# Kernel tuning notes

Hardware: AMD Instinct MI355X
Metric: run time of the kernel (lower is better)

Reference implementation:

```python
import jax, jax.numpy as jnp
import numpy as np

B, C, W, H = 4, 256, 64, 64
CQ = C // 8


def setup_inputs() -> dict:
    key = jax.random.key(0)
    ks = jax.random.split(key, 8)
    s = 1.0 / np.sqrt(C)
    return {
        "x": jax.random.normal(ks[0], (B, C, W, H), dtype=jnp.float32),
        "Wq": jax.random.normal(ks[1], (CQ, C), dtype=jnp.float32) * s,
        "bq": jnp.zeros((CQ,), dtype=jnp.float32),
        "Wk": jax.random.normal(ks[2], (CQ, C), dtype=jnp.float32) * s,
        "bk": jnp.zeros((CQ,), dtype=jnp.float32),
        "Wv": jax.random.normal(ks[3], (C, C), dtype=jnp.float32) * s,
        "bv": jnp.zeros((C,), dtype=jnp.float32),
        "gamma": jnp.zeros((1,), dtype=jnp.float32),
    }


def reference(x, Wq, bq, Wk, bk, Wv, bv, gamma):
    b, c, w, h = x.shape
    n = w * h
    xf = x.reshape(b, c, n)  # [B, C, N] flattened spatial
    # 1x1 convs are channel-wise linear maps
    q = jnp.einsum("dc,bcn->bnd", Wq, xf) + bq  # [B, N, C//8]
    k = jnp.einsum("dc,bcn->bdn", Wk, xf) + bk[None, :, None]  # [B, C//8, N]
    v = jnp.einsum("dc,bcn->bdn", Wv, xf) + bv[None, :, None]  # [B, C, N]
    attn = jax.nn.softmax(jnp.einsum("bnd,bdm->bnm", q, k), axis=-1)  # [B, N, N]
    # out[b, c, n] = sum_m v[b, c, m] * attn[b, n, m]
    out = jnp.einsum("bdm,bnm->bdn", v, attn).reshape(b, c, w, h)
    return gamma[0] * out + x
```

## Files before the change

kernel.cpp:

```cpp
#include <hip/hip_runtime.h>
#include <hip/hip_bf16.h>

#define CC 256
#define NN 4096
#define CQ 32
#define LOG2E 1.4426950408889634f

using short8 = __attribute__((ext_vector_type(8))) short;
using f32x4  = __attribute__((ext_vector_type(4))) float;

static __device__ __forceinline__ short f2bf(float f) {
  __hip_bfloat16 h = __float2bfloat16(f);
  return *reinterpret_cast<short*>(&h);
}

__global__ __launch_bounds__(256) void prep_kernel(
    const float* __restrict__ Wq, const float* __restrict__ Wk,
    const float* __restrict__ Wv, __hip_bfloat16* __restrict__ Wf)
{
  int t = blockIdx.x*256 + threadIdx.x;
  int lane = t & 63, frag = t >> 6;
  int tile = frag >> 3, kc = frag & 7;
  int l15 = lane & 15, quad = lane >> 4;
  int R = tile*16 + l15;
  int k0 = kc*32 + quad*8;
  const float* src;
  if (R < 32)       src = Wq + (size_t)R*CC + k0;
  else if (R < 64)  src = Wk + (size_t)(R-32)*CC + k0;
  else              src = Wv + (size_t)(R-64)*CC + k0;
  float4 a = *(const float4*)(src);
  float4 c = *(const float4*)(src + 4);
  short8 o;
  o[0]=f2bf(a.x); o[1]=f2bf(a.y); o[2]=f2bf(a.z); o[3]=f2bf(a.w);
  o[4]=f2bf(c.x); o[5]=f2bf(c.y); o[6]=f2bf(c.z); o[7]=f2bf(c.w);
  *reinterpret_cast<short8*>(reinterpret_cast<short*>(Wf) + (size_t)t*8) = o;
}

__global__ __launch_bounds__(512, 2) void qkv_kernel(
    const float* __restrict__ x, const __hip_bfloat16* __restrict__ Wf,
    const float* __restrict__ bq, const float* __restrict__ bk,
    const float* __restrict__ bv,
    __hip_bfloat16* __restrict__ qb, __hip_bfloat16* __restrict__ kb,
    __hip_bfloat16* __restrict__ vb)
{
  const int b  = blockIdx.y;
  const int n0 = blockIdx.x * 64;
  const int tid = threadIdx.x;
  const int lane = tid & 63;
  const int w = __builtin_amdgcn_readfirstlane(tid >> 6);
  const int l15 = lane & 15, quad = lane >> 4;

  __shared__ __align__(16) short Xs[64][264];
  __shared__ __align__(16) short Vr[8][16][72];

  const int sn = tid & 63, cg8 = tid >> 6;
  const float* xcol = x + (size_t)b*CC*NN + n0 + sn;
#pragma unroll
  for (int it = 0; it < 4; it++) {
    int cbase = it*64 + cg8*8;
    float v[8];
#pragma unroll
    for (int j = 0; j < 8; j++) v[j] = xcol[(size_t)(cbase + j)*NN];
    short8 sv;
#pragma unroll
    for (int j = 0; j < 8; j++) sv[j] = f2bf(v[j]);
    *reinterpret_cast<short8*>(&Xs[sn][cbase]) = sv;
  }
  __syncthreads();

  const short* wfp = reinterpret_cast<const short*>(Wf);

#define QKV_TILE(T) { \
    const int t_ = (T); \
    short8 Af[8]; \
    _Pragma("unroll") \
    for (int kc = 0; kc < 8; kc++) \
      Af[kc] = *(const short8*)(wfp + ((size_t)(t_*8 + kc)*64 + lane)*8); \
    f32x4 ac0 = {0.f,0.f,0.f,0.f}, ac1 = {0.f,0.f,0.f,0.f}; \
    f32x4 ac2 = {0.f,0.f,0.f,0.f}, ac3 = {0.f,0.f,0.f,0.f}; \
    _Pragma("unroll") \
    for (int kc = 0; kc < 8; kc++) { \
      short8 B0 = *(const short8*)(&Xs[     l15][kc*32 + quad*8]); \
      short8 B1 = *(const short8*)(&Xs[16 + l15][kc*32 + quad*8]); \
      short8 B2 = *(const short8*)(&Xs[32 + l15][kc*32 + quad*8]); \
      short8 B3 = *(const short8*)(&Xs[48 + l15][kc*32 + quad*8]); \
      ac0 = __builtin_amdgcn_mfma_f32_16x16x32_bf16(Af[kc], B0, ac0, 0,0,0); \
      ac1 = __builtin_amdgcn_mfma_f32_16x16x32_bf16(Af[kc], B1, ac1, 0,0,0); \
      ac2 = __builtin_amdgcn_mfma_f32_16x16x32_bf16(Af[kc], B2, ac2, 0,0,0); \
      ac3 = __builtin_amdgcn_mfma_f32_16x16x32_bf16(Af[kc], B3, ac3, 0,0,0); \
    } \
    if (t_ < 2) { \
      int d0 = t_*16; \
      _Pragma("unroll") \
      for (int r = 0; r < 4; r++) { \
        int d = d0 + quad*4 + r; float bb = bq[d]; \
        qb[(size_t)b*NN*CQ + (size_t)(n0      + l15)*CQ + d] = __float2bfloat16(LOG2E*(ac0[r] + bb)); \
        qb[(size_t)b*NN*CQ + (size_t)(n0 + 16 + l15)*CQ + d] = __float2bfloat16(LOG2E*(ac1[r] + bb)); \
        qb[(size_t)b*NN*CQ + (size_t)(n0 + 32 + l15)*CQ + d] = __float2bfloat16(LOG2E*(ac2[r] + bb)); \
        qb[(size_t)b*NN*CQ + (size_t)(n0 + 48 + l15)*CQ + d] = __float2bfloat16(LOG2E*(ac3[r] + bb)); \
      } \
    } else if (t_ < 4) { \
      int d0 = (t_-2)*16; \
      _Pragma("unroll") \
      for (int r = 0; r < 4; r++) { \
        int d = d0 + quad*4 + r; float bb = bk[d]; \
        kb[(size_t)b*NN*CQ + (size_t)(n0      + l15)*CQ + d] = __float2bfloat16(ac0[r] + bb); \
        kb[(size_t)b*NN*CQ + (size_t)(n0 + 16 + l15)*CQ + d] = __float2bfloat16(ac1[r] + bb); \
        kb[(size_t)b*NN*CQ + (size_t)(n0 + 32 + l15)*CQ + d] = __float2bfloat16(ac2[r] + bb); \
        kb[(size_t)b*NN*CQ + (size_t)(n0 + 48 + l15)*CQ + d] = __float2bfloat16(ac3[r] + bb); \
      } \
    } else { \
      int rv0 = (t_-4)*16; \
      _Pragma("unroll") \
      for (int r = 0; r < 4; r++) { \
        float bb = bv[rv0 + quad*4 + r]; \
        Vr[w][quad*4 + r][     l15] = f2bf(ac0[r] + bb); \
        Vr[w][quad*4 + r][16 + l15] = f2bf(ac1[r] + bb); \
        Vr[w][quad*4 + r][32 + l15] = f2bf(ac2[r] + bb); \
        Vr[w][quad*4 + r][48 + l15] = f2bf(ac3[r] + bb); \
      } \
      int row = lane >> 2, cb = (lane & 3)*16; \
      short8 t0 = *(const short8*)(&Vr[w][row][cb]); \
      short8 t1 = *(const short8*)(&Vr[w][row][cb + 8]); \
      *(short8*)(vb + ((size_t)b*CC + rv0 + row)*NN + n0 + cb)     = t0; \
      *(short8*)(vb + ((size_t)b*CC + rv0 + row)*NN + n0 + cb + 8) = t1; \
    } }

  QKV_TILE(2*w);
  QKV_TILE(2*w + 1);
  if (w < 4) { QKV_TILE(16 + w); }
#undef QKV_TILE
}

__global__ __launch_bounds__(512, 2) void attn_kernel(
    const __hip_bfloat16* __restrict__ qb, const __hip_bfloat16* __restrict__ kb,
    const __hip_bfloat16* __restrict__ vb,
    const float* __restrict__ x, const float* __restrict__ gamma,
    float* __restrict__ out)
{
  const int Bk = blockIdx.x;
  const int b = (Bk & 7) >> 1;
  const int n0 = ((Bk >> 3)*2 + (Bk & 1)) * 64;
  const int tid = threadIdx.x;
  const int lane = tid & 63;
  const int w = __builtin_amdgcn_readfirstlane(tid >> 6);
  const int sg = w & 3;
  const int mh = w >> 2;
  const int l15 = lane & 15, quad = lane >> 4;

  __shared__ __align__(16) short Vs[256][72];
  __shared__ __align__(16) short Ps[64][72];
  __shared__ float Lbuf2[2][64];

  const short* qbase = (const short*)qb + (size_t)b*NN*CQ;
  const short* kbase = (const short*)kb + (size_t)b*NN*CQ;
  const short* vbase = (const short*)vb + (size_t)b*CC*NN;

  short8 aq = *(const short8*)(qbase + (size_t)(n0 + sg*16 + l15)*CQ + quad*8);

  const int vr = tid >> 1, sh = tid & 1;

  short8 vf0, vf1, vf2, vf3, kf0, kf1;
#pragma unroll
  for (int j = 0; j < 4; j++) {
    short8 t = *(const short8*)(vbase + (size_t)vr*NN + sh*32 + j*8);
    if (j == 0) vf0 = t; else if (j == 1) vf1 = t; else if (j == 2) vf2 = t; else vf3 = t;
  }
  kf0 = *(const short8*)(kbase + (size_t)(mh*32 +      l15)*CQ + quad*8);
  kf1 = *(const short8*)(kbase + (size_t)(mh*32 + 16 + l15)*CQ + quad*8);
  *(short8*)(&Vs[vr][sh*32 +  0]) = vf0;
  *(short8*)(&Vs[vr][sh*32 +  8]) = vf1;
  *(short8*)(&Vs[vr][sh*32 + 16]) = vf2;
  *(short8*)(&Vs[vr][sh*32 + 24]) = vf3;

  f32x4 acc[4][4];
#pragma unroll
  for (int cg = 0; cg < 4; cg++)
#pragma unroll
    for (int ng = 0; ng < 4; ng++) acc[cg][ng] = (f32x4){0.f,0.f,0.f,0.f};
  float lsum[4] = {0.f,0.f,0.f,0.f};

  __syncthreads();

  for (int T = 0; T < 64; T++) {
    short8 nv0, nv1, nv2, nv3, nk0, nk1;
    if (T < 63) {
      const short* vp = vbase + (size_t)vr*NN + (T+1)*64 + sh*32;
      nv0 = *(const short8*)(vp);
      nv1 = *(const short8*)(vp + 8);
      nv2 = *(const short8*)(vp + 16);
      nv3 = *(const short8*)(vp + 24);
      nk0 = *(const short8*)(kbase + (size_t)((T+1)*64 + mh*32 +      l15)*CQ + quad*8);
      nk1 = *(const short8*)(kbase + (size_t)((T+1)*64 + mh*32 + 16 + l15)*CQ + quad*8);
    }

    f32x4 z = {0.f,0.f,0.f,0.f};
    f32x4 S0 = __builtin_amdgcn_mfma_f32_16x16x32_bf16(aq, kf0, z, 0,0,0);
    f32x4 S1 = __builtin_amdgcn_mfma_f32_16x16x32_bf16(aq, kf1, z, 0,0,0);
#pragma unroll
    for (int r = 0; r < 4; r++) {
      float e0 = __builtin_amdgcn_exp2f(S0[r]);
      float e1 = __builtin_amdgcn_exp2f(S1[r]);
      lsum[r] += e0 + e1;
      Ps[sg*16 + quad*4 + r][mh*32 +      l15] = f2bf(e0);
      Ps[sg*16 + quad*4 + r][mh*32 + 16 + l15] = f2bf(e1);
    }
    __syncthreads();

    short8 ap0 = *(const short8*)(&Ps[     l15][mh*32 + quad*8]);
    short8 ap1 = *(const short8*)(&Ps[16 + l15][mh*32 + quad*8]);
    short8 ap2 = *(const short8*)(&Ps[32 + l15][mh*32 + quad*8]);
    short8 ap3 = *(const short8*)(&Ps[48 + l15][mh*32 + quad*8]);
#pragma unroll
    for (int cg = 0; cg < 4; cg++) {
      short8 av = *(const short8*)(&Vs[sg*64 + cg*16 + l15][mh*32 + quad*8]);
      acc[cg][0] = __builtin_amdgcn_mfma_f32_16x16x32_bf16(av, ap0, acc[cg][0], 0,0,0);
      acc[cg][1] = __builtin_amdgcn_mfma_f32_16x16x32_bf16(av, ap1, acc[cg][1], 0,0,0);
      acc[cg][2] = __builtin_amdgcn_mfma_f32_16x16x32_bf16(av, ap2, acc[cg][2], 0,0,0);
      acc[cg][3] = __builtin_amdgcn_mfma_f32_16x16x32_bf16(av, ap3, acc[cg][3], 0,0,0);
    }
    __syncthreads();

    if (T < 63) {
      *(short8*)(&Vs[vr][sh*32 +  0]) = nv0;
      *(short8*)(&Vs[vr][sh*32 +  8]) = nv1;
      *(short8*)(&Vs[vr][sh*32 + 16]) = nv2;
      *(short8*)(&Vs[vr][sh*32 + 24]) = nv3;
      kf0 = nk0; kf1 = nk1;
    }
  }

#pragma unroll
  for (int r = 0; r < 4; r++) {
    float s = lsum[r];
    s += __shfl_xor(s, 1); s += __shfl_xor(s, 2);
    s += __shfl_xor(s, 4); s += __shfl_xor(s, 8);
    if (l15 == 0) Lbuf2[mh][sg*16 + quad*4 + r] = s;
  }

  float* poolf = reinterpret_cast<float*>(&Vs[0][0]);
  __syncthreads();
#pragma unroll
  for (int g = 0; g < 2; g++) {
    if (mh == 1 && (sg >> 1) == g) {
#pragma unroll
      for (int cg = 0; cg < 4; cg++)
#pragma unroll
        for (int ng = 0; ng < 4; ng++)
#pragma unroll
          for (int r = 0; r < 4; r++)
            poolf[(sg & 1)*4096 + (cg*16 + quad*4 + r)*64 + ng*16 + l15] = acc[cg][ng][r];
    }
    __syncthreads();
    if (mh == 0 && (sg >> 1) == g) {
#pragma unroll
      for (int cg = 0; cg < 4; cg++)
#pragma unroll
        for (int ng = 0; ng < 4; ng++)
#pragma unroll
          for (int r = 0; r < 4; r++)
            acc[cg][ng][r] += poolf[(sg & 1)*4096 + (cg*16 + quad*4 + r)*64 + ng*16 + l15];
    }
    __syncthreads();
  }

  if (mh == 0) {
    const float gm = gamma[0];
    float Lv[4];
#pragma unroll
    for (int ng = 0; ng < 4; ng++)
      Lv[ng] = 1.0f / (Lbuf2[0][ng*16 + l15] + Lbuf2[1][ng*16 + l15]);
#pragma unroll
    for (int cg = 0; cg < 4; cg++) {
#pragma unroll
      for (int ng = 0; ng < 4; ng++) {
#pragma unroll
        for (int r = 0; r < 4; r++) {
          size_t idx = ((size_t)b*CC + sg*64 + cg*16 + quad*4 + r)*NN + n0 + ng*16 + l15;
          out[idx] = gm * acc[cg][ng][r] * Lv[ng] + x[idx];
        }
      }
    }
  }
}

extern "C" void kernel_launch(void* const* d_in, const int* in_sizes, int n_in,
                              void* d_out, int out_size, void* d_ws, size_t ws_size,
                              hipStream_t stream) {
  const float* x     = (const float*)d_in[0];
  const float* Wq    = (const float*)d_in[1];
  const float* bq    = (const float*)d_in[2];
  const float* Wk    = (const float*)d_in[3];
  const float* bk    = (const float*)d_in[4];
  const float* Wv    = (const float*)d_in[5];
  const float* bv    = (const float*)d_in[6];
  const float* gamma = (const float*)d_in[7];
  float* out = (float*)d_out;

  char* ws = (char*)d_ws;
  if (ws_size < (11u << 20)) return;
  __hip_bfloat16* qb = (__hip_bfloat16*)(ws);
  __hip_bfloat16* kb = (__hip_bfloat16*)(ws + (1u << 20));
  __hip_bfloat16* vb = (__hip_bfloat16*)(ws + (2u << 20));
  __hip_bfloat16* Wf = (__hip_bfloat16*)(ws + (10u << 20));

  prep_kernel<<<dim3(40), 256, 0, stream>>>(Wq, Wk, Wv, Wf);
  qkv_kernel<<<dim3(64, 4), 512, 0, stream>>>(x, Wf, bq, bk, bv, qb, kb, vb);
  attn_kernel<<<dim3(256), 512, 0, stream>>>(qb, kb, vb, x, gamma, out);
}
```

Before: 155.1 us.

## Load V fragments directly to registers and double-buffer P to drop a barrier

Each wave now reads its V MFMA operands straight from global memory into registers instead of staging V through shared memory. The P tile is double-buffered in LDS so the exp/score step for tile T+1 overlaps the PV MFMAs for tile T, leaving one barrier per iteration instead of two. The K prefetch is moved two tiles ahead. In exchange, global V loads become strided per lane (rows of NN) and register pressure rises. LDS is reduced to one shared float pool that is reused for the epilogue.

```diff
diff --git a/kernel.cpp b/kernel.cpp
--- a/kernel.cpp
+++ b/kernel.cpp
@@ -148,9 +148,9 @@
   const int mh = w >> 2;
   const int l15 = lane & 15, quad = lane >> 4;
 
-  __shared__ __align__(16) short Vs[256][72];
-  __shared__ __align__(16) short Ps[64][72];
+  __shared__ __align__(16) float poolf[8192];
   __shared__ float Lbuf2[2][64];
+  auto Ps = reinterpret_cast<short (*)[64][72]>(poolf);
 
   const short* qbase = (const short*)qb + (size_t)b*NN*CQ;
   const short* kbase = (const short*)kb + (size_t)b*NN*CQ;
@@ -158,76 +158,93 @@
 
   short8 aq = *(const short8*)(qbase + (size_t)(n0 + sg*16 + l15)*CQ + quad*8);
 
-  const int vr = tid >> 1, sh = tid & 1;
-
-  short8 vf0, vf1, vf2, vf3, kf0, kf1;
-#pragma unroll
-  for (int j = 0; j < 4; j++) {
-    short8 t = *(const short8*)(vbase + (size_t)vr*NN + sh*32 + j*8);
-    if (j == 0) vf0 = t; else if (j == 1) vf1 = t; else if (j == 2) vf2 = t; else vf3 = t;
-  }
-  kf0 = *(const short8*)(kbase + (size_t)(mh*32 +      l15)*CQ + quad*8);
-  kf1 = *(const short8*)(kbase + (size_t)(mh*32 + 16 + l15)*CQ + quad*8);
-  *(short8*)(&Vs[vr][sh*32 +  0]) = vf0;
-  *(short8*)(&Vs[vr][sh*32 +  8]) = vf1;
-  *(short8*)(&Vs[vr][sh*32 + 16]) = vf2;
-  *(short8*)(&Vs[vr][sh*32 + 24]) = vf3;
-
+  const short* vp0 = vbase + (size_t)(sg*64 +      l15)*NN + mh*32 + quad*8;
+  const short* vp1 = vp0 + (size_t)16*NN;
+  const short* vp2 = vp0 + (size_t)32*NN;
+  const short* vp3 = vp0 + (size_t)48*NN;
+  const short* kp0 = kbase + (size_t)(mh*32 +      l15)*CQ + quad*8;
+  const short* kp1 = kbase + (size_t)(mh*32 + 16 + l15)*CQ + quad*8;
+
+  const f32x4 z = {0.f,0.f,0.f,0.f};
   f32x4 acc[4][4];
 #pragma unroll
   for (int cg = 0; cg < 4; cg++)
 #pragma unroll
-    for (int ng = 0; ng < 4; ng++) acc[cg][ng] = (f32x4){0.f,0.f,0.f,0.f};
+    for (int ng = 0; ng < 4; ng++) acc[cg][ng] = z;
   float lsum[4] = {0.f,0.f,0.f,0.f};
 
+  short8 kf0 = *(const short8*)(kp0);
+  short8 kf1 = *(const short8*)(kp1);
+  short8 vf0 = *(const short8*)(vp0);
+  short8 vf1 = *(const short8*)(vp1);
+  short8 vf2 = *(const short8*)(vp2);
+  short8 vf3 = *(const short8*)(vp3);
+  {
+    f32x4 s0 = __builtin_amdgcn_mfma_f32_16x16x32_bf16(aq, kf0, z, 0,0,0);
+    f32x4 s1 = __builtin_amdgcn_mfma_f32_16x16x32_bf16(aq, kf1, z, 0,0,0);
+#pragma unroll
+    for (int r = 0; r < 4; r++) {
+      float e0 = __builtin_amdgcn_exp2f(s0[r]);
+      float e1 = __builtin_amdgcn_exp2f(s1[r]);
+      lsum[r] += e0 + e1;
+      Ps[0][sg*16 + quad*4 + r][mh*32 +      l15] = f2bf(e0);
+      Ps[0][sg*16 + quad*4 + r][mh*32 + 16 + l15] = f2bf(e1);
+    }
+  }
+  kf0 = *(const short8*)(kp0 + 64*CQ);
+  kf1 = *(const short8*)(kp1 + 64*CQ);
   __syncthreads();
 
   for (int T = 0; T < 64; T++) {
-    short8 nv0, nv1, nv2, nv3, nk0, nk1;
+    const int Tn = (T < 63) ? T + 1 : 63;
+    const int Tk = (T < 62) ? T + 2 : 63;
+    short8 nv0 = *(const short8*)(vp0 + Tn*64);
+    short8 nv1 = *(const short8*)(vp1 + Tn*64);
+    short8 nv2 = *(const short8*)(vp2 + Tn*64);
+    short8 nv3 = *(const short8*)(vp3 + Tn*64);
+    short8 nk0 = *(const short8*)(kp0 + (size_t)Tk*64*CQ);
+    short8 nk1 = *(const short8*)(kp1 + (size_t)Tk*64*CQ);
+
+    const int pb = T & 1;
+    short8 ap0 = *(const short8*)(&Ps[pb][     l15][mh*32 + quad*8]);
+    short8 ap1 = *(const short8*)(&Ps[pb][16 + l15][mh*32 + quad*8]);
+    short8 ap2 = *(const short8*)(&Ps[pb][32 + l15][mh*32 + quad*8]);
+    short8 ap3 = *(const short8*)(&Ps[pb][48 + l15][mh*32 + quad*8]);
+
     if (T < 63) {
-      const short* vp = vbase + (size_t)vr*NN + (T+1)*64 + sh*32;
-      nv0 = *(const short8*)(vp);
-      nv1 = *(const short8*)(vp + 8);
-      nv2 = *(const short8*)(vp + 16);
-      nv3 = *(const short8*)(vp + 24);
-      nk0 = *(const short8*)(kbase + (size_t)((T+1)*64 + mh*32 +      l15)*CQ + quad*8);
-      nk1 = *(const short8*)(kbase + (size_t)((T+1)*64 + mh*32 + 16 + l15)*CQ + quad*8);
-    }
-
-    f32x4 z = {0.f,0.f,0.f,0.f};
-    f32x4 S0 = __builtin_amdgcn_mfma_f32_16x16x32_bf16(aq, kf0, z, 0,0,0);
-    f32x4 S1 = __builtin_amdgcn_mfma_f32_16x16x32_bf16(aq, kf1, z, 0,0,0);
-#pragma unroll
-    for (int r = 0; r < 4; r++) {
-      float e0 = __builtin_amdgcn_exp2f(S0[r]);
-      float e1 = __builtin_amdgcn_exp2f(S1[r]);
-      lsum[r] += e0 + e1;
-      Ps[sg*16 + quad*4 + r][mh*32 +      l15] = f2bf(e0);
-      Ps[sg*16 + quad*4 + r][mh*32 + 16 + l15] = f2bf(e1);
-    }
+      f32x4 s0 = __builtin_amdgcn_mfma_f32_16x16x32_bf16(aq, kf0, z, 0,0,0);
+      f32x4 s1 = __builtin_amdgcn_mfma_f32_16x16x32_bf16(aq, kf1, z, 0,0,0);
+#pragma unroll
+      for (int r = 0; r < 4; r++) {
+        float e0 = __builtin_amdgcn_exp2f(s0[r]);
+        float e1 = __builtin_amdgcn_exp2f(s1[r]);
+        lsum[r] += e0 + e1;
+        Ps[pb^1][sg*16 + quad*4 + r][mh*32 +      l15] = f2bf(e0);
+        Ps[pb^1][sg*16 + quad*4 + r][mh*32 + 16 + l15] = f2bf(e1);
+      }
+    }
+
+    acc[0][0] = __builtin_amdgcn_mfma_f32_16x16x32_bf16(vf0, ap0, acc[0][0], 0,0,0);
+    acc[0][1] = __builtin_amdgcn_mfma_f32_16x16x32_bf16(vf0, ap1, acc[0][1], 0,0,0);
+    acc[0][2] = __builtin_amdgcn_mfma_f32_16x16x32_bf16(vf0, ap2, acc[0][2], 0,0,0);
+    acc[0][3] = __builtin_amdgcn_mfma_f32_16x16x32_bf16(vf0, ap3, acc[0][3], 0,0,0);
+    acc[1][0] = __builtin_amdgcn_mfma_f32_16x16x32_bf16(vf1, ap0, acc[1][0], 0,0,0);
+    acc[1][1] = __builtin_amdgcn_mfma_f32_16x16x32_bf16(vf1, ap1, acc[1][1], 0,0,0);
+    acc[1][2] = __builtin_amdgcn_mfma_f32_16x16x32_bf16(vf1, ap2, acc[1][2], 0,0,0);
+    acc[1][3] = __builtin_amdgcn_mfma_f32_16x16x32_bf16(vf1, ap3, acc[1][3], 0,0,0);
+    acc[2][0] = __builtin_amdgcn_mfma_f32_16x16x32_bf16(vf2, ap0, acc[2][0], 0,0,0);
+    acc[2][1] = __builtin_amdgcn_mfma_f32_16x16x32_bf16(vf2, ap1, acc[2][1], 0,0,0);
+    acc[2][2] = __builtin_amdgcn_mfma_f32_16x16x32_bf16(vf2, ap2, acc[2][2], 0,0,0);
+    acc[2][3] = __builtin_amdgcn_mfma_f32_16x16x32_bf16(vf2, ap3, acc[2][3], 0,0,0);
+    acc[3][0] = __builtin_amdgcn_mfma_f32_16x16x32_bf16(vf3, ap0, acc[3][0], 0,0,0);
+    acc[3][1] = __builtin_amdgcn_mfma_f32_16x16x32_bf16(vf3, ap1, acc[3][1], 0,0,0);
+    acc[3][2] = __builtin_amdgcn_mfma_f32_16x16x32_bf16(vf3, ap2, acc[3][2], 0,0,0);
+    acc[3][3] = __builtin_amdgcn_mfma_f32_16x16x32_bf16(vf3, ap3, acc[3][3], 0,0,0);
+
+    vf0 = nv0; vf1 = nv1; vf2 = nv2; vf3 = nv3;
+    kf0 = nk0; kf1 = nk1;
+
     __syncthreads();
-
-    short8 ap0 = *(const short8*)(&Ps[     l15][mh*32 + quad*8]);
-    short8 ap1 = *(const short8*)(&Ps[16 + l15][mh*32 + quad*8]);
-    short8 ap2 = *(const short8*)(&Ps[32 + l15][mh*32 + quad*8]);
-    short8 ap3 = *(const short8*)(&Ps[48 + l15][mh*32 + quad*8]);
-#pragma unroll
-    for (int cg = 0; cg < 4; cg++) {
-      short8 av = *(const short8*)(&Vs[sg*64 + cg*16 + l15][mh*32 + quad*8]);
-      acc[cg][0] = __builtin_amdgcn_mfma_f32_16x16x32_bf16(av, ap0, acc[cg][0], 0,0,0);
-      acc[cg][1] = __builtin_amdgcn_mfma_f32_16x16x32_bf16(av, ap1, acc[cg][1], 0,0,0);
-      acc[cg][2] = __builtin_amdgcn_mfma_f32_16x16x32_bf16(av, ap2, acc[cg][2], 0,0,0);
-      acc[cg][3] = __builtin_amdgcn_mfma_f32_16x16x32_bf16(av, ap3, acc[cg][3], 0,0,0);
-    }
-    __syncthreads();
-
-    if (T < 63) {
-      *(short8*)(&Vs[vr][sh*32 +  0]) = nv0;
-      *(short8*)(&Vs[vr][sh*32 +  8]) = nv1;
-      *(short8*)(&Vs[vr][sh*32 + 16]) = nv2;
-      *(short8*)(&Vs[vr][sh*32 + 24]) = nv3;
-      kf0 = nk0; kf1 = nk1;
-    }
   }
 
 #pragma unroll
@@ -238,7 +255,6 @@
     if (l15 == 0) Lbuf2[mh][sg*16 + quad*4 + r] = s;
   }
 
-  float* poolf = reinterpret_cast<float*>(&Vs[0][0]);
   __syncthreads();
 #pragma unroll
   for (int g = 0; g < 2; g++) {
```

After: 173.4 us. 1.12x slower.

## Double-buffer V and P tiles in LDS to overlap softmax with PV MFMA

Applied to the files above, without the earlier changes.

Splits the V and P shared-memory tiles into two buffers and software-pipelines the loop. Each iteration computes QK^T and exp for the next key tile into the alternate P buffer while running the PV MFMAs on the current one, and the two barriers per iteration become one. This is meant to hide the exp and LDS-store latency and cut barrier stalls. In exchange, LDS use per block roughly doubles, which may lower the number of resident blocks per CU.

```diff
diff --git a/kernel.cpp b/kernel.cpp
--- a/kernel.cpp
+++ b/kernel.cpp
@@ -148,8 +148,8 @@
   const int mh = w >> 2;
   const int l15 = lane & 15, quad = lane >> 4;
 
-  __shared__ __align__(16) short Vs[256][72];
-  __shared__ __align__(16) short Ps[64][72];
+  __shared__ __align__(16) short Vs[2][256][72];
+  __shared__ __align__(16) short Ps[2][64][72];
   __shared__ float Lbuf2[2][64];
 
   const short* qbase = (const short*)qb + (size_t)b*NN*CQ;
@@ -159,75 +159,94 @@
   short8 aq = *(const short8*)(qbase + (size_t)(n0 + sg*16 + l15)*CQ + quad*8);
 
   const int vr = tid >> 1, sh = tid & 1;
-
-  short8 vf0, vf1, vf2, vf3, kf0, kf1;
-#pragma unroll
-  for (int j = 0; j < 4; j++) {
-    short8 t = *(const short8*)(vbase + (size_t)vr*NN + sh*32 + j*8);
-    if (j == 0) vf0 = t; else if (j == 1) vf1 = t; else if (j == 2) vf2 = t; else vf3 = t;
-  }
-  kf0 = *(const short8*)(kbase + (size_t)(mh*32 +      l15)*CQ + quad*8);
-  kf1 = *(const short8*)(kbase + (size_t)(mh*32 + 16 + l15)*CQ + quad*8);
-  *(short8*)(&Vs[vr][sh*32 +  0]) = vf0;
-  *(short8*)(&Vs[vr][sh*32 +  8]) = vf1;
-  *(short8*)(&Vs[vr][sh*32 + 16]) = vf2;
-  *(short8*)(&Vs[vr][sh*32 + 24]) = vf3;
-
+  const short* vrow = vbase + (size_t)vr*NN + sh*32;
+
+  const f32x4 z = {0.f,0.f,0.f,0.f};
   f32x4 acc[4][4];
 #pragma unroll
   for (int cg = 0; cg < 4; cg++)
 #pragma unroll
-    for (int ng = 0; ng < 4; ng++) acc[cg][ng] = (f32x4){0.f,0.f,0.f,0.f};
+    for (int ng = 0; ng < 4; ng++) acc[cg][ng] = z;
   float lsum[4] = {0.f,0.f,0.f,0.f};
 
+  {
+    short8 a0 = *(const short8*)(vrow);
+    short8 a1 = *(const short8*)(vrow + 8);
+    short8 a2 = *(const short8*)(vrow + 16);
+    short8 a3 = *(const short8*)(vrow + 24);
+    *(short8*)(&Vs[0][vr][sh*32 +  0]) = a0;
+    *(short8*)(&Vs[0][vr][sh*32 +  8]) = a1;
+    *(short8*)(&Vs[0][vr][sh*32 + 16]) = a2;
+    *(short8*)(&Vs[0][vr][sh*32 + 24]) = a3;
+  }
+  {
+    short8 k00 = *(const short8*)(kbase + (size_t)(mh*32 +      l15)*CQ + quad*8);
+    short8 k01 = *(const short8*)(kbase + (size_t)(mh*32 + 16 + l15)*CQ + quad*8);
+    f32x4 s0 = __builtin_amdgcn_mfma_f32_16x16x32_bf16(aq, k00, z, 0,0,0);
+    f32x4 s1 = __builtin_amdgcn_mfma_f32_16x16x32_bf16(aq, k01, z, 0,0,0);
+#pragma unroll
+    for (int r = 0; r < 4; r++) {
+      float e0 = __builtin_amdgcn_exp2f(s0[r]);
+      float e1 = __builtin_amdgcn_exp2f(s1[r]);
+      lsum[r] += e0 + e1;
+      Ps[0][sg*16 + quad*4 + r][mh*32 +      l15] = f2bf(e0);
+      Ps[0][sg*16 + quad*4 + r][mh*32 + 16 + l15] = f2bf(e1);
+    }
+  }
+  short8 kf0 = *(const short8*)(kbase + (size_t)(64 + mh*32 +      l15)*CQ + quad*8);
+  short8 kf1 = *(const short8*)(kbase + (size_t)(64 + mh*32 + 16 + l15)*CQ + quad*8);
   __syncthreads();
 
   for (int T = 0; T < 64; T++) {
-    short8 nv0, nv1, nv2, nv3, nk0, nk1;
+    const int cur = T & 1;
+
+    short8 nv0, nv1, nv2, nv3;
     if (T < 63) {
-      const short* vp = vbase + (size_t)vr*NN + (T+1)*64 + sh*32;
+      const short* vp = vrow + (size_t)(T+1)*64;
       nv0 = *(const short8*)(vp);
       nv1 = *(const short8*)(vp + 8);
       nv2 = *(const short8*)(vp + 16);
       nv3 = *(const short8*)(vp + 24);
-      nk0 = *(const short8*)(kbase + (size_t)((T+1)*64 + mh*32 +      l15)*CQ + quad*8);
-      nk1 = *(const short8*)(kbase + (size_t)((T+1)*64 + mh*32 + 16 + l15)*CQ + quad*8);
-    }
-
-    f32x4 z = {0.f,0.f,0.f,0.f};
-    f32x4 S0 = __builtin_amdgcn_mfma_f32_16x16x32_bf16(aq, kf0, z, 0,0,0);
-    f32x4 S1 = __builtin_amdgcn_mfma_f32_16x16x32_bf16(aq, kf1, z, 0,0,0);
-#pragma unroll
-    for (int r = 0; r < 4; r++) {
-      float e0 = __builtin_amdgcn_exp2f(S0[r]);
-      float e1 = __builtin_amdgcn_exp2f(S1[r]);
-      lsum[r] += e0 + e1;
-      Ps[sg*16 + quad*4 + r][mh*32 +      l15] = f2bf(e0);
-      Ps[sg*16 + quad*4 + r][mh*32 + 16 + l15] = f2bf(e1);
-    }
-    __syncthreads();
-
-    short8 ap0 = *(const short8*)(&Ps[     l15][mh*32 + quad*8]);
-    short8 ap1 = *(const short8*)(&Ps[16 + l15][mh*32 + quad*8]);
-    short8 ap2 = *(const short8*)(&Ps[32 + l15][mh*32 + quad*8]);
-    short8 ap3 = *(const short8*)(&Ps[48 + l15][mh*32 + quad*8]);
+    }
+
+    short8 ap0 = *(const short8*)(&Ps[cur][     l15][mh*32 + quad*8]);
+    short8 ap1 = *(const short8*)(&Ps[cur][16 + l15][mh*32 + quad*8]);
+    short8 ap2 = *(const short8*)(&Ps[cur][32 + l15][mh*32 + quad*8]);
+    short8 ap3 = *(const short8*)(&Ps[cur][48 + l15][mh*32 + quad*8]);
+
+    if (T < 63) {
+      f32x4 s0 = __builtin_amdgcn_mfma_f32_16x16x32_bf16(aq, kf0, z, 0,0,0);
+      f32x4 s1 = __builtin_amdgcn_mfma_f32_16x16x32_bf16(aq, kf1, z, 0,0,0);
+#pragma unroll
+      for (int r = 0; r < 4; r++) {
+        float e0 = __builtin_amdgcn_exp2f(s0[r]);
+        float e1 = __builtin_amdgcn_exp2f(s1[r]);
+        lsum[r] += e0 + e1;
+        Ps[cur^1][sg*16 + quad*4 + r][mh*32 +      l15] = f2bf(e0);
+        Ps[cur^1][sg*16 + quad*4 + r][mh*32 + 16 + l15] = f2bf(e1);
+      }
+      const int Tk = (T + 2 <= 63) ? T + 2 : 63;
+      kf0 = *(const short8*)(kbase + (size_t)(Tk*64 + mh*32 +      l15)*CQ + quad*8);
+      kf1 = *(const short8*)(kbase + (size_t)(Tk*64 + mh*32 + 16 + l15)*CQ + quad*8);
+    }
+
 #pragma unroll
     for (int cg = 0; cg < 4; cg++) {
-      short8 av = *(const short8*)(&Vs[sg*64 + cg*16 + l15][mh*32 + quad*8]);
+      short8 av = *(const short8*)(&Vs[cur][sg*64 + cg*16 + l15][mh*32 + quad*8]);
       acc[cg][0] = __builtin_amdgcn_mfma_f32_16x16x32_bf16(av, ap0, acc[cg][0], 0,0,0);
       acc[cg][1] = __builtin_amdgcn_mfma_f32_16x16x32_bf16(av, ap1, acc[cg][1], 0,0,0);
       acc[cg][2] = __builtin_amdgcn_mfma_f32_16x16x32_bf16(av, ap2, acc[cg][2], 0,0,0);
       acc[cg][3] = __builtin_amdgcn_mfma_f32_16x16x32_bf16(av, ap3, acc[cg][3], 0,0,0);
     }
+
+    if (T < 63) {
+      *(short8*)(&Vs[cur^1][vr][sh*32 +  0]) = nv0;
+      *(short8*)(&Vs[cur^1][vr][sh*32 +  8]) = nv1;
+      *(short8*)(&Vs[cur^1][vr][sh*32 + 16]) = nv2;
+      *(short8*)(&Vs[cur^1][vr][sh*32 + 24]) = nv3;
+    }
+
     __syncthreads();
-
-    if (T < 63) {
-      *(short8*)(&Vs[vr][sh*32 +  0]) = nv0;
-      *(short8*)(&Vs[vr][sh*32 +  8]) = nv1;
-      *(short8*)(&Vs[vr][sh*32 + 16]) = nv2;
-      *(short8*)(&Vs[vr][sh*32 + 24]) = nv3;
-      kf0 = nk0; kf1 = nk1;
-    }
   }
 
 #pragma unroll
@@ -238,7 +257,7 @@
     if (l15 == 0) Lbuf2[mh][sg*16 + quad*4 + r] = s;
   }
 
-  float* poolf = reinterpret_cast<float*>(&Vs[0][0]);
+  float* poolf = reinterpret_cast<float*>(&Vs[0][0][0]);
   __syncthreads();
 #pragma unroll
   for (int g = 0; g < 2; g++) {
```

Measured after the change: 174.7 us. 12.7% more time.

## Halve attention query tile to 32 rows with 4-wave blocks and 512 blocks

Applied to the files above, without the earlier changes.

The attention kernel now handles 32 query positions per block with 256 threads instead of 64 with 512, which doubles the grid to 512 blocks. Each wave accumulates 8x2 output tiles covering 128 channels, and the cross-wave reduction drops to a single pass. Padding of the shared V and P rows changes from 72 to 76 to alter the bank mapping. The intent is to give the GPU's many CUs more blocks to schedule. The cost is that each K/V tile is reloaded by twice as many blocks, doubling global/L2 traffic for V.

```diff
diff --git a/kernel.cpp b/kernel.cpp
--- a/kernel.cpp
+++ b/kernel.cpp
@@ -132,7 +132,7 @@
 #undef QKV_TILE
 }
 
-__global__ __launch_bounds__(512, 2) void attn_kernel(
+__global__ __launch_bounds__(256, 2) void attn_kernel(
     const __hip_bfloat16* __restrict__ qb, const __hip_bfloat16* __restrict__ kb,
     const __hip_bfloat16* __restrict__ vb,
     const float* __restrict__ x, const float* __restrict__ gamma,
@@ -140,17 +140,18 @@
 {
   const int Bk = blockIdx.x;
   const int b = (Bk & 7) >> 1;
-  const int n0 = ((Bk >> 3)*2 + (Bk & 1)) * 64;
+  const int nt = (Bk >> 3)*2 + (Bk & 1);
+  const int n0 = nt * 32;
   const int tid = threadIdx.x;
   const int lane = tid & 63;
   const int w = __builtin_amdgcn_readfirstlane(tid >> 6);
-  const int sg = w & 3;
-  const int mh = w >> 2;
+  const int sg = w & 1;
+  const int mh = w >> 1;
   const int l15 = lane & 15, quad = lane >> 4;
 
-  __shared__ __align__(16) short Vs[256][72];
-  __shared__ __align__(16) short Ps[64][72];
-  __shared__ float Lbuf2[2][64];
+  __shared__ __align__(16) short Vs[256][76];
+  __shared__ __align__(16) short Ps[32][76];
+  __shared__ float Lbuf2[2][32];
 
   const short* qbase = (const short*)qb + (size_t)b*NN*CQ;
   const short* kbase = (const short*)kb + (size_t)b*NN*CQ;
@@ -158,43 +159,38 @@
 
   short8 aq = *(const short8*)(qbase + (size_t)(n0 + sg*16 + l15)*CQ + quad*8);
 
-  const int vr = tid >> 1, sh = tid & 1;
-
-  short8 vf0, vf1, vf2, vf3, kf0, kf1;
-#pragma unroll
-  for (int j = 0; j < 4; j++) {
-    short8 t = *(const short8*)(vbase + (size_t)vr*NN + sh*32 + j*8);
-    if (j == 0) vf0 = t; else if (j == 1) vf1 = t; else if (j == 2) vf2 = t; else vf3 = t;
-  }
-  kf0 = *(const short8*)(kbase + (size_t)(mh*32 +      l15)*CQ + quad*8);
-  kf1 = *(const short8*)(kbase + (size_t)(mh*32 + 16 + l15)*CQ + quad*8);
-  *(short8*)(&Vs[vr][sh*32 +  0]) = vf0;
-  *(short8*)(&Vs[vr][sh*32 +  8]) = vf1;
-  *(short8*)(&Vs[vr][sh*32 + 16]) = vf2;
-  *(short8*)(&Vs[vr][sh*32 + 24]) = vf3;
-
-  f32x4 acc[4][4];
-#pragma unroll
-  for (int cg = 0; cg < 4; cg++)
-#pragma unroll
-    for (int ng = 0; ng < 4; ng++) acc[cg][ng] = (f32x4){0.f,0.f,0.f,0.f};
+  const int vr = tid;
+  const short* vrow = vbase + (size_t)vr*NN;
+
+  const f32x4 z = {0.f,0.f,0.f,0.f};
+  f32x4 acc[8][2];
+#pragma unroll
+  for (int cg = 0; cg < 8; cg++)
+#pragma unroll
+    for (int ng = 0; ng < 2; ng++) acc[cg][ng] = z;
   float lsum[4] = {0.f,0.f,0.f,0.f};
 
+  {
+    short8 sv[8];
+#pragma unroll
+    for (int j = 0; j < 8; j++) sv[j] = *(const short8*)(vrow + j*8);
+#pragma unroll
+    for (int j = 0; j < 8; j++) *(short8*)(&Vs[vr][j*8]) = sv[j];
+  }
+  short8 kf0 = *(const short8*)(kbase + (size_t)(mh*32 +      l15)*CQ + quad*8);
+  short8 kf1 = *(const short8*)(kbase + (size_t)(mh*32 + 16 + l15)*CQ + quad*8);
   __syncthreads();
 
   for (int T = 0; T < 64; T++) {
-    short8 nv0, nv1, nv2, nv3, nk0, nk1;
+    short8 nv[8]; short8 nk0, nk1;
     if (T < 63) {
-      const short* vp = vbase + (size_t)vr*NN + (T+1)*64 + sh*32;
-      nv0 = *(const short8*)(vp);
-      nv1 = *(const short8*)(vp + 8);
-      nv2 = *(const short8*)(vp + 16);
-      nv3 = *(const short8*)(vp + 24);
+      const short* vp = vrow + (size_t)(T+1)*64;
+#pragma unroll
+      for (int j = 0; j < 8; j++) nv[j] = *(const short8*)(vp + j*8);
       nk0 = *(const short8*)(kbase + (size_t)((T+1)*64 + mh*32 +      l15)*CQ + quad*8);
       nk1 = *(const short8*)(kbase + (size_t)((T+1)*64 + mh*32 + 16 + l15)*CQ + quad*8);
     }
 
-    f32x4 z = {0.f,0.f,0.f,0.f};
     f32x4 S0 = __builtin_amdgcn_mfma_f32_16x16x32_bf16(aq, kf0, z, 0,0,0);
     f32x4 S1 = __builtin_amdgcn_mfma_f32_16x16x32_bf16(aq, kf1, z, 0,0,0);
 #pragma unroll
@@ -209,23 +205,17 @@
 
     short8 ap0 = *(const short8*)(&Ps[     l15][mh*32 + quad*8]);
     short8 ap1 = *(const short8*)(&Ps[16 + l15][mh*32 + quad*8]);
-    short8 ap2 = *(const short8*)(&Ps[32 + l15][mh*32 + quad*8]);
-    short8 ap3 = *(const short8*)(&Ps[48 + l15][mh*32 + quad*8]);
-#pragma unroll
-    for (int cg = 0; cg < 4; cg++) {
-      short8 av = *(const short8*)(&Vs[sg*64 + cg*16 + l15][mh*32 + quad*8]);
+#pragma unroll
+    for (int cg = 0; cg < 8; cg++) {
+      short8 av = *(const short8*)(&Vs[sg*128 + cg*16 + l15][mh*32 + quad*8]);
       acc[cg][0] = __builtin_amdgcn_mfma_f32_16x16x32_bf16(av, ap0, acc[cg][0], 0,0,0);
       acc[cg][1] = __builtin_amdgcn_mfma_f32_16x16x32_bf16(av, ap1, acc[cg][1], 0,0,0);
-      acc[cg][2] = __builtin_amdgcn_mfma_f32_16x16x32_bf16(av, ap2, acc[cg][2], 0,0,0);
-      acc[cg][3] = __builtin_amdgcn_mfma_f32_16x16x32_bf16(av, ap3, acc[cg][3], 0,0,0);
     }
     __syncthreads();
 
     if (T < 63) {
-      *(short8*)(&Vs[vr][sh*32 +  0]) = nv0;
-      *(short8*)(&Vs[vr][sh*32 +  8]) = nv1;
-      *(short8*)(&Vs[vr][sh*32 + 16]) = nv2;
-      *(short8*)(&Vs[vr][sh*32 + 24]) = nv3;
+#pragma unroll
+      for (int j = 0; j < 8; j++) *(short8*)(&Vs[vr][j*8]) = nv[j];
       kf0 = nk0; kf1 = nk1;
     }
   }
@@ -240,43 +230,39 @@
 
   float* poolf = reinterpret_cast<float*>(&Vs[0][0]);
   __syncthreads();
-#pragma unroll
-  for (int g = 0; g < 2; g++) {
-    if (mh == 1 && (sg >> 1) == g) {
-#pragma unroll
-      for (int cg = 0; cg < 4; cg++)
-#pragma unroll
-        for (int ng = 0; ng < 4; ng++)
-#pragma unroll
-          for (int r = 0; r < 4; r++)
-            poolf[(sg & 1)*4096 + (cg*16 + quad*4 + r)*64 + ng*16 + l15] = acc[cg][ng][r];
-    }
-    __syncthreads();
-    if (mh == 0 && (sg >> 1) == g) {
-#pragma unroll
-      for (int cg = 0; cg < 4; cg++)
-#pragma unroll
-        for (int ng = 0; ng < 4; ng++)
-#pragma unroll
-          for (int r = 0; r < 4; r++)
-            acc[cg][ng][r] += poolf[(sg & 1)*4096 + (cg*16 + quad*4 + r)*64 + ng*16 + l15];
-    }
-    __syncthreads();
+  if (mh == 1) {
+#pragma unroll
+    for (int cg = 0; cg < 8; cg++)
+#pragma unroll
+      for (int ng = 0; ng < 2; ng++)
+#pragma unroll
+        for (int r = 0; r < 4; r++)
+          poolf[sg*4096 + (cg*16 + quad*4 + r)*32 + ng*16 + l15] = acc[cg][ng][r];
+  }
+  __syncthreads();
+  if (mh == 0) {
+#pragma unroll
+    for (int cg = 0; cg < 8; cg++)
+#pragma unroll
+      for (int ng = 0; ng < 2; ng++)
+#pragma unroll
+        for (int r = 0; r < 4; r++)
+          acc[cg][ng][r] += poolf[sg*4096 + (cg*16 + quad*4 + r)*32 + ng*16 + l15];
   }
 
   if (mh == 0) {
     const float gm = gamma[0];
-    float Lv[4];
-#pragma unroll
-    for (int ng = 0; ng < 4; ng++)
+    float Lv[2];
+#pragma unroll
+    for (int ng = 0; ng < 2; ng++)
       Lv[ng] = 1.0f / (Lbuf2[0][ng*16 + l15] + Lbuf2[1][ng*16 + l15]);
 #pragma unroll
-    for (int cg = 0; cg < 4; cg++) {
-#pragma unroll
-      for (int ng = 0; ng < 4; ng++) {
+    for (int cg = 0; cg < 8; cg++) {
+#pragma unroll
+      for (int ng = 0; ng < 2; ng++) {
 #pragma unroll
         for (int r = 0; r < 4; r++) {
-          size_t idx = ((size_t)b*CC + sg*64 + cg*16 + quad*4 + r)*NN + n0 + ng*16 + l15;
+          size_t idx = ((size_t)b*CC + sg*128 + cg*16 + quad*4 + r)*NN + n0 + ng*16 + l15;
           out[idx] = gm * acc[cg][ng][r] * Lv[ng] + x[idx];
         }
       }
@@ -306,5 +292,5 @@
 
   prep_kernel<<<dim3(40), 256, 0, stream>>>(Wq, Wk, Wv, Wf);
   qkv_kernel<<<dim3(64, 4), 512, 0, stream>>>(x, Wf, bq, bk, bv, qb, kb, vb);
-  attn_kernel<<<dim3(256), 512, 0, stream>>>(qb, kb, vb, x, gamma, out);
-}
+  attn_kernel<<<dim3(512), 256, 0, stream>>>(qb, kb, vb, x, gamma, out);
+}
```

Result: slower. 230.9 us (+48.9%).
